# Kernel tuning notes

Hardware: AMD Instinct MI355X
Metric: run time of the kernel (lower is better)

The kernel has to match this reference:

```python
import jax, jax.numpy as jnp
import numpy as np
from jax.scipy.linalg import expm

B, T, D = 4096, 256, 64


def setup_inputs() -> dict:
    key = jax.random.key(0)
    k1, k2, k3 = jax.random.split(key, 3)
    inputs = jax.random.normal(k1, (B, T, D), dtype=jnp.float32)
    time = jax.random.uniform(k2, (T,), dtype=jnp.float32)  # TIME grid in [0,1)
    kernel = jax.random.normal(k3, (D, D), dtype=jnp.float32) * 0.1  # learned Koopman generator
    return {"inputs": inputs, "time": time, "kernel": kernel}


def reference(inputs, time, kernel):
    # expm(kernel * t) for every t, batched instead of a Python loop: [T, D, D]
    mats = jax.vmap(lambda t: expm(kernel * t))(time)
    # original: einsum('ijk,lk->lij', mats, inputs[:, 0, :]) -> [B, T, D]
    x0 = inputs[:, 0, :]  # [B, D] initial condition
    trajs = jnp.einsum('tij,bj->bti', mats, x0)
    return trajs
```

## Files before the change

kernel.cpp:

```cpp
#include <hip/hip_runtime.h>
#include <math.h>


#define TT 256
#define DD 64
#define BB 4096
#define S1 68
#define THETA 0.5f
#define MTERMS 10

typedef __attribute__((ext_vector_type(8))) short short8;
typedef __attribute__((ext_vector_type(4))) float f32x4;

__device__ __forceinline__ void bf16_split(float x, unsigned short& hi, unsigned short& lo) {
    union { float f; unsigned int u; } a; a.f = x;
    unsigned int r = (a.u + 0x7fffu + ((a.u >> 16) & 1u)) & 0xffff0000u;
    hi = (unsigned short)(r >> 16);
    union { float f; unsigned int u; } d; d.f = x - __uint_as_float(r);
    lo = (unsigned short)(d.u >> 16);
}


__device__ __forceinline__ void mm68(const float* __restrict__ Lt,
                                     const float* __restrict__ R,
                                     float* __restrict__ C,
                                     float f, float* __restrict__ Eacc, int tid) {
    const int i0 = (tid & 15) * 4;
    const int j0 = (tid >> 4) * 4;
    float acc[4][4];
#pragma unroll
    for (int r = 0; r < 4; ++r)
#pragma unroll
        for (int c = 0; c < 4; ++c) acc[r][c] = 0.f;

#pragma unroll 8
    for (int k = 0; k < 64; ++k) {
        const float4 a = *reinterpret_cast<const float4*>(&Lt[k * S1 + i0]);
        const float4 b = *reinterpret_cast<const float4*>(&R[k * S1 + j0]);
        const float av[4] = {a.x, a.y, a.z, a.w};
        const float bv[4] = {b.x, b.y, b.z, b.w};
#pragma unroll
        for (int r = 0; r < 4; ++r)
#pragma unroll
            for (int c = 0; c < 4; ++c) acc[r][c] = fmaf(av[r], bv[c], acc[r][c]);
    }

#pragma unroll
    for (int r = 0; r < 4; ++r) {
        float4 v;
        v.x = acc[r][0] * f; v.y = acc[r][1] * f; v.z = acc[r][2] * f; v.w = acc[r][3] * f;
        *reinterpret_cast<float4*>(&C[(i0 + r) * S1 + j0]) = v;
        if (Eacc) {
            float* e = &Eacc[(i0 + r) * S1 + j0];
            e[0] += v.x; e[1] += v.y; e[2] += v.z; e[3] += v.w;
        }
    }
}

__device__ __forceinline__ void transpose68(const float* __restrict__ X,
                                            float* __restrict__ XT, int tid) {
    const int i = tid >> 2;
    const int j0 = (tid & 3) * 16;
#pragma unroll
    for (int c4 = 0; c4 < 4; ++c4) {
        const float4 v = *reinterpret_cast<const float4*>(&X[i * S1 + j0 + 4 * c4]);
        XT[(j0 + 4 * c4 + 0) * S1 + i] = v.x;
        XT[(j0 + 4 * c4 + 1) * S1 + i] = v.y;
        XT[(j0 + 4 * c4 + 2) * S1 + i] = v.z;
        XT[(j0 + 4 * c4 + 3) * S1 + i] = v.w;
    }
}

__global__ __launch_bounds__(256)
void expm_kernel(const float* __restrict__ K, const float* __restrict__ tim,
                 const float* __restrict__ inputs,
                 unsigned short* __restrict__ Bh, unsigned short* __restrict__ Bl,
                 unsigned short* __restrict__ Ah, unsigned short* __restrict__ Al) {
    __shared__ float As[64 * S1];
    __shared__ float Pa[64 * S1];
    __shared__ float Pb[64 * S1];
    __shared__ float Et[64 * S1];
    __shared__ float Tx[64 * S1];
    __shared__ float red[64];

    const int tid = threadIdx.x;
    const int t = blockIdx.x;
    const float tval = tim[t];

    {
        const int idx = t * 1024 + tid * 4;
        const int b = idx >> 6;
        const int j = idx & 63;
        const float4 v = *reinterpret_cast<const float4*>(inputs + (size_t)b * (TT * DD) + j);
        ushort4 h, l;
        bf16_split(v.x, h.x, l.x); bf16_split(v.y, h.y, l.y);
        bf16_split(v.z, h.z, l.z); bf16_split(v.w, h.w, l.w);
        *reinterpret_cast<ushort4*>(&Ah[b * 64 + j]) = h;
        *reinterpret_cast<ushort4*>(&Al[b * 64 + j]) = l;
    }

    if (tid < 64) {
        float s = 0.f;
        for (int j = 0; j < 64; ++j) s += fabsf(K[tid * 64 + j]);
        red[tid] = s;
    }
    __syncthreads();
    if (tid == 0) {
        float m = 0.f;
        for (int i = 0; i < 64; ++i) m = fmaxf(m, red[i]);
        const float nt = m * tval;
        int s = 0;
        if (nt > THETA) {
            s = (int)ceilf(log2f(nt / THETA));
            if (s < 0) s = 0;
        }
        red[0] = ldexpf(tval, -s);
        red[1] = (float)s;
    }
    __syncthreads();
    const float scale = red[0];
    const int sq = (int)red[1];
    __syncthreads();

    {
        const int i = tid >> 2;
        const int j0 = (tid & 3) * 16;
#pragma unroll
        for (int c = 0; c < 16; ++c) {
            const int j = j0 + c;
            const float v = K[i * 64 + j] * scale;
            As[i * S1 + j] = v;
            Pa[j * S1 + i] = v;
            Et[j * S1 + i] = v + ((i == j) ? 1.f : 0.f);
        }
    }
    __syncthreads();

    float* Pcur = Pa;
    float* Pnext = Pb;
    for (int n = 2; n <= MTERMS; ++n) {
        mm68(As, Pcur, Pnext, 1.0f / (float)n, Et, tid);
        __syncthreads();
        float* tmp = Pcur; Pcur = Pnext; Pnext = tmp;
    }

    transpose68(Et, Tx, tid);
    __syncthreads();
    float* cur = Tx;
    float* nxt = Pa;
    const float* curT = Et;
    for (int r = 0; r < sq; ++r) {
        if (r > 0) {
            transpose68(cur, Pb, tid);
            __syncthreads();
            curT = Pb;
        }
        mm68(curT, cur, nxt, 1.f, nullptr, tid);
        __syncthreads();
        float* tmp = cur; cur = nxt; nxt = tmp;
    }

    {
        const int i = tid >> 2;
        const int j0 = (tid & 3) * 16;
        unsigned short* oh = Bh + (size_t)t * 4096 + i * 64 + j0;
        unsigned short* ol = Bl + (size_t)t * 4096 + i * 64 + j0;
#pragma unroll
        for (int c4 = 0; c4 < 4; ++c4) {
            const float4 v = *reinterpret_cast<const float4*>(&cur[i * S1 + j0 + 4 * c4]);
            ushort4 h, l;
            bf16_split(v.x, h.x, l.x); bf16_split(v.y, h.y, l.y);
            bf16_split(v.z, h.z, l.z); bf16_split(v.w, h.w, l.w);
            *reinterpret_cast<ushort4*>(oh + 4 * c4) = h;
            *reinterpret_cast<ushort4*>(ol + 4 * c4) = l;
        }
    }
}


__global__ __launch_bounds__(256)
void traj_mfma(const unsigned short* __restrict__ Ah, const unsigned short* __restrict__ Al,
               const unsigned short* __restrict__ Bh, const unsigned short* __restrict__ Bl,
               float* __restrict__ out) {
    const int tid = threadIdx.x;
    const int t  = blockIdx.x & (TT - 1);
    const int bg = blockIdx.x >> 8;
    const int w  = tid >> 6;
    const int l  = tid & 63;
    const int ln = l & 15;
    const int qd = l >> 4;

    const unsigned short* mh = Bh + (size_t)t * 4096;
    const unsigned short* ml = Bl + (size_t)t * 4096;
    short8 Mh[4][2], Ml[4][2];
#pragma unroll
    for (int m = 0; m < 4; ++m)
#pragma unroll
        for (int kh = 0; kh < 2; ++kh) {
            const int off = (m * 16 + ln) * 64 + kh * 32 + qd * 8;
            Mh[m][kh] = *reinterpret_cast<const short8*>(mh + off);
            Ml[m][kh] = *reinterpret_cast<const short8*>(ml + off);
        }

    const int brow0 = bg * 256 + w * 64;
#pragma unroll
    for (int it = 0; it < 4; ++it) {
        const int brow = brow0 + it * 16 + ln;

        short8 Xh[2], Xl[2];
#pragma unroll
        for (int kh = 0; kh < 2; ++kh) {
            const int aoff = brow * 64 + kh * 32 + qd * 8;
            Xh[kh] = *reinterpret_cast<const short8*>(Ah + aoff);
            Xl[kh] = *reinterpret_cast<const short8*>(Al + aoff);
        }

        f32x4 acc[4];
#pragma unroll
        for (int m = 0; m < 4; ++m) acc[m] = (f32x4){0.f, 0.f, 0.f, 0.f};

#pragma unroll
        for (int kh = 0; kh < 2; ++kh)
#pragma unroll
            for (int m = 0; m < 4; ++m) {
                acc[m] = __builtin_amdgcn_mfma_f32_16x16x32_bf16(Mh[m][kh], Xh[kh], acc[m], 0, 0, 0);
                acc[m] = __builtin_amdgcn_mfma_f32_16x16x32_bf16(Ml[m][kh], Xh[kh], acc[m], 0, 0, 0);
                acc[m] = __builtin_amdgcn_mfma_f32_16x16x32_bf16(Mh[m][kh], Xl[kh], acc[m], 0, 0, 0);
            }

        float* obase = out + (size_t)brow * (TT * DD) + (size_t)t * DD + qd * 4;
#pragma unroll
        for (int m = 0; m < 4; ++m) {
            float4 v;
            v.x = acc[m][0]; v.y = acc[m][1]; v.z = acc[m][2]; v.w = acc[m][3];
            *reinterpret_cast<float4*>(obase + m * 16) = v;
        }
    }
}

extern "C" void kernel_launch(void* const* d_in, const int* in_sizes, int n_in,
                              void* d_out, int out_size, void* d_ws, size_t ws_size,
                              hipStream_t stream) {
    const float* inputs = (const float*)d_in[0];
    const float* tim    = (const float*)d_in[1];
    const float* K      = (const float*)d_in[2];
    float* out = (float*)d_out;

    unsigned short* Bh = (unsigned short*)d_ws;
    unsigned short* Bl = Bh + (size_t)TT * DD * DD;
    unsigned short* Ah = Bl + (size_t)TT * DD * DD;
    unsigned short* Al = Ah + (size_t)BB * DD;

    expm_kernel<<<TT, 256, 0, stream>>>(K, tim, inputs, Bh, Bl, Ah, Al);
    traj_mfma<<<(BB / 256) * TT, 256, 0, stream>>>(Ah, Al, Bh, Bl, out);
}
```

Baseline: 447.7 us.

## Fuse expm and trajectory MFMA into one kernel, relax Taylor parameters

Merges the matrix-exponential kernel and the trajectory GEMM kernel so each time-step block converts its result from shared memory directly into MFMA fragments and streams all batch rows, removing the workspace round-trip and the second launch. It also raises the scaling threshold and drops one Taylor term to cut squarings and matrix products. The cost is far fewer blocks doing the 256MB output write, which lowers occupancy and latency hiding, plus repeated reads of the inputs per block; the looser Taylor settings may reduce accuracy.

Result: no change. 449.1 us (+0.3%).

```diff
diff --git a/kernel.cpp b/kernel.cpp
--- a/kernel.cpp
+++ b/kernel.cpp
@@ -6,8 +6,8 @@
 #define DD 64
 #define BB 4096
 #define S1 68
-#define THETA 0.5f
-#define MTERMS 10
+#define THETA 1.0f
+#define MTERMS 9
 
 typedef __attribute__((ext_vector_type(8))) short short8;
 typedef __attribute__((ext_vector_type(4))) float f32x4;
@@ -19,7 +19,6 @@
     union { float f; unsigned int u; } d; d.f = x - __uint_as_float(r);
     lo = (unsigned short)(d.u >> 16);
 }
-
 
 __device__ __forceinline__ void mm68(const float* __restrict__ Lt,
                                      const float* __restrict__ R,
@@ -72,10 +71,8 @@
 }
 
 __global__ __launch_bounds__(256)
-void expm_kernel(const float* __restrict__ K, const float* __restrict__ tim,
-                 const float* __restrict__ inputs,
-                 unsigned short* __restrict__ Bh, unsigned short* __restrict__ Bl,
-                 unsigned short* __restrict__ Ah, unsigned short* __restrict__ Al) {
+void expm_traj(const float* __restrict__ K, const float* __restrict__ tim,
+               const float* __restrict__ inputs, float* __restrict__ out) {
     __shared__ float As[64 * S1];
     __shared__ float Pa[64 * S1];
     __shared__ float Pb[64 * S1];
@@ -86,18 +83,6 @@
     const int tid = threadIdx.x;
     const int t = blockIdx.x;
     const float tval = tim[t];
-
-    {
-        const int idx = t * 1024 + tid * 4;
-        const int b = idx >> 6;
-        const int j = idx & 63;
-        const float4 v = *reinterpret_cast<const float4*>(inputs + (size_t)b * (TT * DD) + j);
-        ushort4 h, l;
-        bf16_split(v.x, h.x, l.x); bf16_split(v.y, h.y, l.y);
-        bf16_split(v.z, h.z, l.z); bf16_split(v.w, h.w, l.w);
-        *reinterpret_cast<ushort4*>(&Ah[b * 64 + j]) = h;
-        *reinterpret_cast<ushort4*>(&Al[b * 64 + j]) = l;
-    }
 
     if (tid < 64) {
         float s = 0.f;
@@ -160,59 +145,48 @@
         float* tmp = cur; cur = nxt; nxt = tmp;
     }
 
-    {
-        const int i = tid >> 2;
-        const int j0 = (tid & 3) * 16;
-        unsigned short* oh = Bh + (size_t)t * 4096 + i * 64 + j0;
-        unsigned short* ol = Bl + (size_t)t * 4096 + i * 64 + j0;
-#pragma unroll
-        for (int c4 = 0; c4 < 4; ++c4) {
-            const float4 v = *reinterpret_cast<const float4*>(&cur[i * S1 + j0 + 4 * c4]);
-            ushort4 h, l;
-            bf16_split(v.x, h.x, l.x); bf16_split(v.y, h.y, l.y);
-            bf16_split(v.z, h.z, l.z); bf16_split(v.w, h.w, l.w);
-            *reinterpret_cast<ushort4*>(oh + 4 * c4) = h;
-            *reinterpret_cast<ushort4*>(ol + 4 * c4) = l;
-        }
-    }
-}
-
-
-__global__ __launch_bounds__(256)
-void traj_mfma(const unsigned short* __restrict__ Ah, const unsigned short* __restrict__ Al,
-               const unsigned short* __restrict__ Bh, const unsigned short* __restrict__ Bl,
-               float* __restrict__ out) {
-    const int tid = threadIdx.x;
-    const int t  = blockIdx.x & (TT - 1);
-    const int bg = blockIdx.x >> 8;
     const int w  = tid >> 6;
     const int l  = tid & 63;
     const int ln = l & 15;
     const int qd = l >> 4;
 
-    const unsigned short* mh = Bh + (size_t)t * 4096;
-    const unsigned short* ml = Bl + (size_t)t * 4096;
     short8 Mh[4][2], Ml[4][2];
 #pragma unroll
     for (int m = 0; m < 4; ++m)
 #pragma unroll
         for (int kh = 0; kh < 2; ++kh) {
-            const int off = (m * 16 + ln) * 64 + kh * 32 + qd * 8;
-            Mh[m][kh] = *reinterpret_cast<const short8*>(mh + off);
-            Ml[m][kh] = *reinterpret_cast<const short8*>(ml + off);
-        }
-
-    const int brow0 = bg * 256 + w * 64;
-#pragma unroll
-    for (int it = 0; it < 4; ++it) {
-        const int brow = brow0 + it * 16 + ln;
+            const float* src = &cur[(m * 16 + ln) * S1 + kh * 32 + qd * 8];
+            const float4 v0 = *reinterpret_cast<const float4*>(src);
+            const float4 v1 = *reinterpret_cast<const float4*>(src + 4);
+            unsigned short h[8], lo[8];
+            bf16_split(v0.x, h[0], lo[0]); bf16_split(v0.y, h[1], lo[1]);
+            bf16_split(v0.z, h[2], lo[2]); bf16_split(v0.w, h[3], lo[3]);
+            bf16_split(v1.x, h[4], lo[4]); bf16_split(v1.y, h[5], lo[5]);
+            bf16_split(v1.z, h[6], lo[6]); bf16_split(v1.w, h[7], lo[7]);
+            short8 sh, sl;
+#pragma unroll
+            for (int e = 0; e < 8; ++e) { sh[e] = (short)h[e]; sl[e] = (short)lo[e]; }
+            Mh[m][kh] = sh; Ml[m][kh] = sl;
+        }
+
+    for (int it = 0; it < 64; ++it) {
+        const int brow = it * 64 + w * 16 + ln;
 
         short8 Xh[2], Xl[2];
 #pragma unroll
         for (int kh = 0; kh < 2; ++kh) {
-            const int aoff = brow * 64 + kh * 32 + qd * 8;
-            Xh[kh] = *reinterpret_cast<const short8*>(Ah + aoff);
-            Xl[kh] = *reinterpret_cast<const short8*>(Al + aoff);
+            const float* src = inputs + (size_t)brow * (TT * DD) + kh * 32 + qd * 8;
+            const float4 v0 = *reinterpret_cast<const float4*>(src);
+            const float4 v1 = *reinterpret_cast<const float4*>(src + 4);
+            unsigned short h[8], lo[8];
+            bf16_split(v0.x, h[0], lo[0]); bf16_split(v0.y, h[1], lo[1]);
+            bf16_split(v0.z, h[2], lo[2]); bf16_split(v0.w, h[3], lo[3]);
+            bf16_split(v1.x, h[4], lo[4]); bf16_split(v1.y, h[5], lo[5]);
+            bf16_split(v1.z, h[6], lo[6]); bf16_split(v1.w, h[7], lo[7]);
+            short8 sh, sl;
+#pragma unroll
+            for (int e = 0; e < 8; ++e) { sh[e] = (short)h[e]; sl[e] = (short)lo[e]; }
+            Xh[kh] = sh; Xl[kh] = sl;
         }
 
         f32x4 acc[4];
@@ -245,12 +219,7 @@
     const float* tim    = (const float*)d_in[1];
     const float* K      = (const float*)d_in[2];
     float* out = (float*)d_out;
-
-    unsigned short* Bh = (unsigned short*)d_ws;
-    unsigned short* Bl = Bh + (size_t)TT * DD * DD;
-    unsigned short* Ah = Bl + (size_t)TT * DD * DD;
-    unsigned short* Al = Ah + (size_t)BB * DD;
-
-    expm_kernel<<<TT, 256, 0, stream>>>(K, tim, inputs, Bh, Bl, Ah, Al);
-    traj_mfma<<<(BB / 256) * TT, 256, 0, stream>>>(Ah, Al, Bh, Bl, out);
-}
+    (void)d_ws; (void)ws_size;
+
+    expm_traj<<<TT, 256, 0, stream>>>(K, tim, inputs, out);
+}
```
